# Optimization experiments

Hardware: AMD Instinct MI355X
Metric: run time of the kernel (lower is better)

## Reference

```python
import jax, jax.numpy as jnp
import numpy as np

B, D_IN = 8192, 512
M0, M1 = 128, 128          # num_modules per layer
K = 8                      # topk (== module_arch[0])
H = 128                    # module hidden (module_arch[1])
T = 4                      # num_tasks
OUT = 2                    # output_dim


def setup_inputs() -> dict:
    key = jax.random.key(0)
    ks = jax.random.split(key, 16)
    s = 0.1
    return {
        "x": jax.random.normal(ks[0], (B, D_IN), jnp.float32),
        "task_id": 1,
        # routing embeddings: [num_tasks, input_dim_of_layer, num_modules]
        "emb0": jax.random.normal(ks[1], (T, D_IN, M0), jnp.float32),
        "emb1": jax.random.normal(ks[2], (T, M0, M1), jnp.float32),
        "emb_out": jax.random.normal(ks[3], (T, M1, 1), jnp.float32),
        # per-module MLP params, stacked over modules: Linear(K->H), Linear(H->1)
        "W1_0": jax.random.normal(ks[4], (M0, K, H), jnp.float32) * s,
        "b1_0": jax.random.normal(ks[5], (M0, H), jnp.float32) * s,
        "W2_0": jax.random.normal(ks[6], (M0, H), jnp.float32) * s,
        "b2_0": jax.random.normal(ks[7], (M0,), jnp.float32) * s,
        "W1_1": jax.random.normal(ks[8], (M1, K, H), jnp.float32) * s,
        "b1_1": jax.random.normal(ks[9], (M1, H), jnp.float32) * s,
        "W2_1": jax.random.normal(ks[10], (M1, H), jnp.float32) * s,
        "b2_1": jax.random.normal(ks[11], (M1,), jnp.float32) * s,
    }


def _topk_masks(emb, k, task_id):
    # emb: [T, D, M]; hard top-k one-hot masks along D (eval path of gumbel_sigmoid,
    # use_gumbel=False, hard=True). Returns [M, k, D] for the given task.
    et = jnp.transpose(emb[task_id], (1, 0))          # [M, D]
    _, idx = jax.lax.top_k(et, k)                     # [M, k]
    return jax.nn.one_hot(idx, et.shape[-1], dtype=emb.dtype)  # [M, k, D]


def _layer(x, emb, W1, b1, W2, b2, task_id):
    masks = _topk_masks(emb, K, task_id)              # [M, K, D]
    inp = jnp.einsum('bd,mkd->bmk', x, masks)         # gather routed inputs
    h = jax.nn.relu(jnp.einsum('bmk,mkh->bmh', inp, W1) + b1)  # [B, M, H]
    return jnp.einsum('bmh,mh->bm', h, W2) + b2       # [B, M]


def reference(x, task_id, emb0, emb1, emb_out,
              W1_0, b1_0, W2_0, b2_0, W1_1, b1_1, W2_1, b2_1):
    x = _layer(x, emb0, W1_0, b1_0, W2_0, b2_0, task_id)
    x = _layer(x, emb1, W1_1, b1_1, W2_1, b2_1, task_id)
    m = _topk_masks(emb_out, OUT, task_id)            # [1, OUT, M1]
    v1 = x @ m[0, 0]                                  # [B]
    v2 = x @ m[0, 1]
    return jax.nn.sigmoid(jnp.stack([v1, v2], axis=1))  # [B, 2]
```

## Files before the change

### kernel.cpp

```cpp
#include <hip/hip_runtime.h>
#include <math.h>

#define B_SZ   8192
#define D_IN   512
#define M0_N   128
#define M1_N   128
#define K_TOP  8
#define H_DIM  128
#define ROWS   16
#define XP     520


template<int NCH>
__device__ __forceinline__ void wave_topk(const float* __restrict__ base,
                                          int stride, int k, int* out_idx,
                                          int lane) {
  float v[NCH];
#pragma unroll
  for (int t = 0; t < NCH; ++t) v[t] = base[(t * 64 + lane) * stride];
  for (int r = 0; r < k; ++r) {
    float bv = -INFINITY;
    int bd = 0x7fffffff;
#pragma unroll
    for (int t = 0; t < NCH; ++t) {
      if (v[t] > bv) { bv = v[t]; bd = t * 64 + lane; }
    }
#pragma unroll
    for (int m = 1; m < 64; m <<= 1) {
      float ov = __shfl_xor(bv, m, 64);
      int   od = __shfl_xor(bd, m, 64);
      if (ov > bv || (ov == bv && od < bd)) { bv = ov; bd = od; }
    }
    if (lane == 0) out_idx[r] = bd;
    if ((bd & 63) == lane) {
      const int tw = bd >> 6;
#pragma unroll
      for (int tt = 0; tt < NCH; ++tt)
        if (tt == tw) v[tt] = -INFINITY;
    }
  }
}

__global__ __launch_bounds__(256)
void route_pre(const int* __restrict__ task_id_p,
               const float* __restrict__ emb0,
               const float* __restrict__ emb1,
               const float* __restrict__ emb_out,
               int* __restrict__ ws) {
  const int task = task_id_p[0];
  const int lane = threadIdx.x & 63;
  const int wid  = threadIdx.x >> 6;
  const int col  = blockIdx.x * 4 + wid;
  if (blockIdx.y == 0) {
    wave_topk<2>(emb1 + (size_t)task * M0_N * M1_N + col, M1_N, K_TOP,
                 ws + 64 + col * 8, lane);
    if (blockIdx.x == 0 && wid == 0)
      wave_topk<2>(emb_out + task * M1_N, 1, 2, ws, lane);
  } else {
    wave_topk<8>(emb0 + (size_t)task * D_IN * M0_N + col, M0_N, K_TOP,
                 ws + 2048 + col * 8, lane);
  }
}

__device__ __forceinline__ float dpp_add16(float p) {
  int t;
  t = __builtin_amdgcn_update_dpp(0, __float_as_int(p), 0xB1, 0xF, 0xF, true);
  p += __int_as_float(t);
  t = __builtin_amdgcn_update_dpp(0, __float_as_int(p), 0x4E, 0xF, 0xF, true);
  p += __int_as_float(t);
  t = __builtin_amdgcn_update_dpp(0, __float_as_int(p), 0x124, 0xF, 0xF, true);
  p += __int_as_float(t);
  t = __builtin_amdgcn_update_dpp(0, __float_as_int(p), 0x128, 0xF, 0xF, true);
  p += __int_as_float(t);
  return p;
}

__device__ __forceinline__ float slice8(const float4* w1a, const float4* w1b,
                                        const float4& b1a, const float4& b1b,
                                        const float4& w2a, const float4& w2b,
                                        const float* xv) {
  float4 h0 = b1a, h1 = b1b;
#pragma unroll
  for (int k = 0; k < 8; ++k) {
    h0.x = fmaf(xv[k], w1a[k].x, h0.x);
    h0.y = fmaf(xv[k], w1a[k].y, h0.y);
    h0.z = fmaf(xv[k], w1a[k].z, h0.z);
    h0.w = fmaf(xv[k], w1a[k].w, h0.w);
    h1.x = fmaf(xv[k], w1b[k].x, h1.x);
    h1.y = fmaf(xv[k], w1b[k].y, h1.y);
    h1.z = fmaf(xv[k], w1b[k].z, h1.z);
    h1.w = fmaf(xv[k], w1b[k].w, h1.w);
  }
  float pa = 0.f, pb = 0.f;
  pa = fmaf(fmaxf(h0.x, 0.f), w2a.x, pa);
  pa = fmaf(fmaxf(h0.y, 0.f), w2a.y, pa);
  pa = fmaf(fmaxf(h0.z, 0.f), w2a.z, pa);
  pa = fmaf(fmaxf(h0.w, 0.f), w2a.w, pa);
  pb = fmaf(fmaxf(h1.x, 0.f), w2b.x, pb);
  pb = fmaf(fmaxf(h1.y, 0.f), w2b.y, pb);
  pb = fmaf(fmaxf(h1.z, 0.f), w2b.z, pb);
  pb = fmaf(fmaxf(h1.w, 0.f), w2b.w, pb);
  return dpp_add16(pa + pb);
}

__global__ __launch_bounds__(256)
void fused_compute(const float* __restrict__ x,
                   const float* __restrict__ W1_0, const float* __restrict__ b1_0,
                   const float* __restrict__ W2_0, const float* __restrict__ b2_0,
                   const float* __restrict__ W1_1, const float* __restrict__ b1_1,
                   const float* __restrict__ W2_1, const float* __restrict__ b2_1,
                   const int* __restrict__ ws, float* __restrict__ out) {
  __shared__ float xt[ROWS * XP];
  __shared__ int   s_m1[2];
  __shared__ int   s_m0[16];
  __shared__ int   s_cols[128];
  __shared__ float tile[16 * 18];

  const int tid = threadIdx.x;
  const int rowbase = blockIdx.x * ROWS;

  float4 xr[8];
#pragma unroll
  for (int i = 0; i < 8; ++i) {
    const int e = tid + i * 256;
    xr[i] = *(const float4*)(x + (size_t)(rowbase + (e >> 7)) * D_IN +
                             (e & 127) * 4);
  }

  if (tid < 128) {
    const int slot = tid >> 3, k = tid & 7;
    const int m1 = ws[slot >> 3];
    const int m0 = ws[64 + m1 * 8 + (slot & 7)];
    if (k == 0) s_m0[slot] = m0;
    s_cols[tid] = ws[2048 + m0 * 8 + k];
    if (tid < 2) s_m1[tid] = ws[tid];
  }

#pragma unroll
  for (int i = 0; i < 8; ++i) {
    const int e = tid + i * 256;
    *(float4*)(xt + (e >> 7) * XP + (e & 127) * 4) = xr[i];
  }
  __syncthreads();

  const int wid  = tid >> 6;
  const int lane = tid & 63;
  const int g    = lane & 15;
  const int rq   = lane >> 4;

#pragma unroll
  for (int si = 0; si < 4; ++si) {
    const int s  = wid * 4 + si;
    const int m0 = s_m0[s];
    const float4* w1p = (const float4*)(W1_0 + (size_t)m0 * (K_TOP * H_DIM));
    float4 w1a[8], w1b[8];
#pragma unroll
    for (int k = 0; k < 8; ++k) {
      w1a[k] = w1p[k * 32 + 2 * g];
      w1b[k] = w1p[k * 32 + 2 * g + 1];
    }
    const float4 b1a = ((const float4*)(b1_0 + m0 * H_DIM))[2 * g];
    const float4 b1b = ((const float4*)(b1_0 + m0 * H_DIM))[2 * g + 1];
    const float4 w2a = ((const float4*)(W2_0 + m0 * H_DIM))[2 * g];
    const float4 w2b = ((const float4*)(W2_0 + m0 * H_DIM))[2 * g + 1];
    const float  b2v = b2_0[m0];
    int cols[8];
#pragma unroll
    for (int k = 0; k < 8; ++k) cols[k] = s_cols[s * 8 + k];

#pragma unroll
    for (int it = 0; it < 4; ++it) {
      const int r = it * 4 + rq;
      const float* xrow = xt + r * XP;
      float xv[8];
#pragma unroll
      for (int k = 0; k < 8; ++k) xv[k] = xrow[cols[k]];
      const float p = slice8(w1a, w1b, b1a, b1b, w2a, w2b, xv);
      if (g == 0) tile[s * 18 + r] = p + b2v;
    }
  }
  __syncthreads();

  {
    const int j  = wid & 1;
    const int rh = wid >> 1;
    const int m1 = s_m1[j];
    const float4* w1p = (const float4*)(W1_1 + (size_t)m1 * (K_TOP * H_DIM));
    float4 w1a[8], w1b[8];
#pragma unroll
    for (int k = 0; k < 8; ++k) {
      w1a[k] = w1p[k * 32 + 2 * g];
      w1b[k] = w1p[k * 32 + 2 * g + 1];
    }
    const float4 b1a = ((const float4*)(b1_1 + m1 * H_DIM))[2 * g];
    const float4 b1b = ((const float4*)(b1_1 + m1 * H_DIM))[2 * g + 1];
    const float4 w2a = ((const float4*)(W2_1 + m1 * H_DIM))[2 * g];
    const float4 w2b = ((const float4*)(W2_1 + m1 * H_DIM))[2 * g + 1];
    const float  b2v = b2_1[m1];

#pragma unroll
    for (int it = 0; it < 2; ++it) {
      const int r = rh * 8 + it * 4 + rq;
      float xv[8];
#pragma unroll
      for (int k = 0; k < 8; ++k) xv[k] = tile[(j * 8 + k) * 18 + r];
      const float p = slice8(w1a, w1b, b1a, b1b, w2a, w2b, xv);
      if (g == 0) {
        const float v = p + b2v;
        out[(size_t)(rowbase + r) * 2 + j] = 1.f / (1.f + __expf(-v));
      }
    }
  }
}

extern "C" void kernel_launch(void* const* d_in, const int* in_sizes, int n_in,
                              void* d_out, int out_size, void* d_ws, size_t ws_size,
                              hipStream_t stream) {
  const float* x       = (const float*)d_in[0];
  const int*   task_id = (const int*)  d_in[1];
  const float* emb0    = (const float*)d_in[2];
  const float* emb1    = (const float*)d_in[3];
  const float* emb_out = (const float*)d_in[4];
  const float* W1_0    = (const float*)d_in[5];
  const float* b1_0    = (const float*)d_in[6];
  const float* W2_0    = (const float*)d_in[7];
  const float* b2_0    = (const float*)d_in[8];
  const float* W1_1    = (const float*)d_in[9];
  const float* b1_1    = (const float*)d_in[10];
  const float* W2_1    = (const float*)d_in[11];
  const float* b2_1    = (const float*)d_in[12];

  int* ws = (int*)d_ws;

  route_pre<<<dim3(32, 2), 256, 0, stream>>>(task_id, emb0, emb1, emb_out, ws);
  fused_compute<<<B_SZ / ROWS, 256, 0, stream>>>(x, W1_0, b1_0, W2_0, b2_0,
                                                 W1_1, b1_1, W2_1, b2_1,
                                                 ws, (float*)d_out);
}
```

Measured before the change: 24.16 us.

## Merge routing top-k and compute into one cooperative kernel with grid sync

Replaces the separate routing kernel and compute kernel with a single cooperative launch of 512 blocks. In each block, wave 0 runs a top-k routing task while the other three waves load the x tile into shared memory. A grid-wide sync then publishes the routing results before the compute phase. This removes one kernel launch and the gap between kernels, and overlaps the x loads with routing. In exchange it adds a grid barrier, needs all 512 blocks co-resident (launch_bounds raised to 2 blocks per CU), and depends on cooperative launch overhead.

```diff
diff --git a/kernel.cpp b/kernel.cpp
--- a/kernel.cpp
+++ b/kernel.cpp
@@ -1,5 +1,8 @@
 #include <hip/hip_runtime.h>
+#include <hip/hip_cooperative_groups.h>
 #include <math.h>
+
+namespace cg = cooperative_groups;
 
 #define B_SZ   8192
 #define D_IN   512
@@ -38,27 +41,6 @@
       for (int tt = 0; tt < NCH; ++tt)
         if (tt == tw) v[tt] = -INFINITY;
     }
-  }
-}
-
-__global__ __launch_bounds__(256)
-void route_pre(const int* __restrict__ task_id_p,
-               const float* __restrict__ emb0,
-               const float* __restrict__ emb1,
-               const float* __restrict__ emb_out,
-               int* __restrict__ ws) {
-  const int task = task_id_p[0];
-  const int lane = threadIdx.x & 63;
-  const int wid  = threadIdx.x >> 6;
-  const int col  = blockIdx.x * 4 + wid;
-  if (blockIdx.y == 0) {
-    wave_topk<2>(emb1 + (size_t)task * M0_N * M1_N + col, M1_N, K_TOP,
-                 ws + 64 + col * 8, lane);
-    if (blockIdx.x == 0 && wid == 0)
-      wave_topk<2>(emb_out + task * M1_N, 1, 2, ws, lane);
-  } else {
-    wave_topk<8>(emb0 + (size_t)task * D_IN * M0_N + col, M0_N, K_TOP,
-                 ws + 2048 + col * 8, lane);
   }
 }
 
@@ -103,29 +85,58 @@
   return dpp_add16(pa + pb);
 }
 
-__global__ __launch_bounds__(256)
-void fused_compute(const float* __restrict__ x,
-                   const float* __restrict__ W1_0, const float* __restrict__ b1_0,
-                   const float* __restrict__ W2_0, const float* __restrict__ b2_0,
-                   const float* __restrict__ W1_1, const float* __restrict__ b1_1,
-                   const float* __restrict__ W2_1, const float* __restrict__ b2_1,
-                   const int* __restrict__ ws, float* __restrict__ out) {
-  __shared__ float xt[ROWS * XP];
+__global__ __launch_bounds__(256, 2)
+void mono(const float* __restrict__ x,
+          const int* __restrict__ task_id_p,
+          const float* __restrict__ emb0,
+          const float* __restrict__ emb1,
+          const float* __restrict__ emb_out,
+          const float* __restrict__ W1_0, const float* __restrict__ b1_0,
+          const float* __restrict__ W2_0, const float* __restrict__ b2_0,
+          const float* __restrict__ W1_1, const float* __restrict__ b1_1,
+          const float* __restrict__ W2_1, const float* __restrict__ b2_1,
+          int* __restrict__ ws, float* __restrict__ out) {
+  __shared__ __align__(16) float xt[ROWS * XP];
   __shared__ int   s_m1[2];
   __shared__ int   s_m0[16];
   __shared__ int   s_cols[128];
   __shared__ float tile[16 * 18];
 
-  const int tid = threadIdx.x;
-  const int rowbase = blockIdx.x * ROWS;
-
-  float4 xr[8];
-#pragma unroll
-  for (int i = 0; i < 8; ++i) {
-    const int e = tid + i * 256;
-    xr[i] = *(const float4*)(x + (size_t)(rowbase + (e >> 7)) * D_IN +
-                             (e & 127) * 4);
-  }
+  const int tid  = threadIdx.x;
+  const int b    = blockIdx.x;
+  const int wid  = tid >> 6;
+  const int lane = tid & 63;
+  const int rowbase = b * ROWS;
+  const int task = task_id_p[0];
+
+  if (wid != 0) {
+    const int li = tid - 64;
+    float4 xr[11];
+#pragma unroll
+    for (int i = 0; i < 11; ++i) {
+      const int e = li + i * 192;
+      if (e < 2048)
+        xr[i] = *(const float4*)(x + (size_t)(rowbase + (e >> 7)) * D_IN +
+                                 (e & 127) * 4);
+    }
+#pragma unroll
+    for (int i = 0; i < 11; ++i) {
+      const int e = li + i * 192;
+      if (e < 2048)
+        *(float4*)(xt + (e >> 7) * XP + (e & 127) * 4) = xr[i];
+    }
+  } else if (b < 128) {
+    wave_topk<2>(emb1 + (size_t)task * M0_N * M1_N + b, M1_N, K_TOP,
+                 ws + 64 + b * 8, lane);
+  } else if (b < 256) {
+    const int col = b - 128;
+    wave_topk<8>(emb0 + (size_t)task * D_IN * M0_N + col, M0_N, K_TOP,
+                 ws + 2048 + col * 8, lane);
+  } else if (b == 256) {
+    wave_topk<2>(emb_out + task * M1_N, 1, 2, ws, lane);
+  }
+
+  cg::this_grid().sync();
 
   if (tid < 128) {
     const int slot = tid >> 3, k = tid & 7;
@@ -135,18 +146,10 @@
     s_cols[tid] = ws[2048 + m0 * 8 + k];
     if (tid < 2) s_m1[tid] = ws[tid];
   }
-
-#pragma unroll
-  for (int i = 0; i < 8; ++i) {
-    const int e = tid + i * 256;
-    *(float4*)(xt + (e >> 7) * XP + (e & 127) * 4) = xr[i];
-  }
   __syncthreads();
 
-  const int wid  = tid >> 6;
-  const int lane = tid & 63;
-  const int g    = lane & 15;
-  const int rq   = lane >> 4;
+  const int g  = lane & 15;
+  const int rq = lane >> 4;
 
 #pragma unroll
   for (int si = 0; si < 4; ++si) {
@@ -230,10 +233,15 @@
   const float* W2_1    = (const float*)d_in[11];
   const float* b2_1    = (const float*)d_in[12];
 
-  int* ws = (int*)d_ws;
-
-  route_pre<<<dim3(32, 2), 256, 0, stream>>>(task_id, emb0, emb1, emb_out, ws);
-  fused_compute<<<B_SZ / ROWS, 256, 0, stream>>>(x, W1_0, b1_0, W2_0, b2_0,
-                                                 W1_1, b1_1, W2_1, b2_1,
-                                                 ws, (float*)d_out);
-}
+  int*   ws  = (int*)d_ws;
+  float* out = (float*)d_out;
+
+  void* args[] = {
+    (void*)&x, (void*)&task_id, (void*)&emb0, (void*)&emb1, (void*)&emb_out,
+    (void*)&W1_0, (void*)&b1_0, (void*)&W2_0, (void*)&b2_0,
+    (void*)&W1_1, (void*)&b1_1, (void*)&W2_1, (void*)&b2_1,
+    (void*)&ws, (void*)&out,
+  };
+  hipLaunchCooperativeKernel((const void*)mono, dim3(B_SZ / ROWS), dim3(256),
+                             args, 0, stream);
+}
```

Result: slower. 81.35 us (+236.7%).
